# Optimization experiments

Hardware: AMD Instinct MI355X
Metric: run time of the kernel (lower is better)

The kernel has to match this reference:

```python
import jax, jax.numpy as jnp
import numpy as np

N_NODES = 50000
N_EDGES = 1600000
NEG_SLOPE = 0.2


def setup_inputs() -> dict:
    key = jax.random.key(0)
    ks = jax.random.split(key, 11)
    s = 0.1  # small init scale
    return {
        "x": jax.random.normal(ks[0], (N_NODES, 128), dtype=jnp.float32),
        "edge_index": jax.random.randint(ks[1], (2, N_EDGES), 0, N_NODES, dtype=jnp.int64),
        "W1": jax.random.normal(ks[2], (128, 128), dtype=jnp.float32) * s,
        "att_src1": jax.random.normal(ks[3], (2, 64), dtype=jnp.float32) * s,
        "att_dst1": jax.random.normal(ks[4], (2, 64), dtype=jnp.float32) * s,
        "b1": jax.random.normal(ks[5], (128,), dtype=jnp.float32) * s,
        "W2": jax.random.normal(ks[6], (128, 64), dtype=jnp.float32) * s,
        "att_src2": jax.random.normal(ks[7], (1, 64), dtype=jnp.float32) * s,
        "att_dst2": jax.random.normal(ks[8], (1, 64), dtype=jnp.float32) * s,
        "b2": jax.random.normal(ks[9], (64,), dtype=jnp.float32) * s,
    }


def gat_conv(x, W, a_src, a_dst, bias, src, dst, n_nodes):
    # x: [N, F_in]; W: [F_in, H*C]; a_src/a_dst: [H, C]; bias: [H*C]
    H, C = a_src.shape
    xl = (x @ W).reshape(n_nodes, H, C)                 # [N,H,C]
    alpha_s = jnp.einsum('nhc,hc->nh', xl, a_src)       # [N,H]
    alpha_d = jnp.einsum('nhc,hc->nh', xl, a_dst)       # [N,H]
    e = jax.nn.leaky_relu(alpha_s[src] + alpha_d[dst], NEG_SLOPE)  # [E,H]
    # segment softmax over edges sharing the same destination node
    m = jax.ops.segment_max(e, dst, num_segments=n_nodes)          # [N,H]
    m = jnp.where(jnp.isfinite(m), m, 0.0)
    e = jnp.exp(e - m[dst])
    denom = jax.ops.segment_sum(e, dst, num_segments=n_nodes)      # [N,H]
    alpha = e / denom[dst]                               # self-loops guarantee denom > 0
    msg = xl[src] * alpha[:, :, None]                    # [E,H,C]
    out = jax.ops.segment_sum(msg, dst, num_segments=n_nodes)      # [N,H,C]
    return out.reshape(n_nodes, H * C) + bias


def reference(x, edge_index, W1, att_src1, att_dst1, b1, W2, att_src2, att_dst2, b2):
    n = x.shape[0]
    # PyG GATConv default add_self_loops=True
    loops = jnp.arange(n, dtype=edge_index.dtype)
    src = jnp.concatenate([edge_index[0], loops])
    dst = jnp.concatenate([edge_index[1], loops])

    h = gat_conv(x, W1, att_src1, att_dst1, b1, src, dst, n)   # [N, 128]
    h = jax.nn.relu(h)                                          # dropout p=0 (eval)
    h = gat_conv(h, W2, att_src2, att_dst2, b2, src, dst, n)   # [N, 64]
    h = jax.nn.relu(h)
    return h
```

## Files before the change

kernel.cpp:

```cpp
#include <hip/hip_runtime.h>
#include <cstdint>
#include <cstddef>

#define NEG_SLOPE 0.2f

#define NB 512
#define LOG_NB 9
#define MAXK 512

__device__ inline unsigned short f2bf(float f) {
    unsigned int u = __float_as_uint(f);
    u += 0x7FFFu + ((u >> 16) & 1u);
    return (unsigned short)(u >> 16);
}
__device__ inline float bf_lo(unsigned int u) { return __uint_as_float(u << 16); }
__device__ inline float bf_hi(unsigned int u) { return __uint_as_float(u & 0xFFFF0000u); }
__device__ inline unsigned int pk2bf(float lo, float hi) {
    return (unsigned int)f2bf(lo) | ((unsigned int)f2bf(hi) << 16);
}

__global__ __launch_bounds__(256) void sort_count_kernel(const int* __restrict__ ei, int E,
                                                         int K, int CH, int* __restrict__ bcnt) {
    __shared__ int hist[MAXK];
    int tid = threadIdx.x;
    for (int i = tid; i < K; i += 256) hist[i] = 0;
    __syncthreads();
    int lo = blockIdx.x * CH;
    int hi = lo + CH; if (hi > E) hi = E;
    for (int e = lo + tid; e < hi; e += 256)
        atomicAdd(&hist[ei[(size_t)E + e] >> LOG_NB], 1);
    __syncthreads();
    for (int i = tid; i < K; i += 256)
        if (hist[i]) atomicAdd(&bcnt[i], hist[i]);
}

__global__ void sort_scan_kernel(const int* __restrict__ bcnt, int* __restrict__ boff,
                                 int* __restrict__ bcur, int K, int E) {
    __shared__ int buf[MAXK];
    int tid = threadIdx.x;
    int v = (tid < K) ? bcnt[tid] : 0;
    buf[tid] = v;
    __syncthreads();
    for (int o = 1; o < MAXK; o <<= 1) {
        int t = (tid >= o) ? buf[tid - o] : 0;
        __syncthreads();
        buf[tid] += t;
        __syncthreads();
    }
    if (tid < K) {
        int ex = buf[tid] - v;
        boff[tid] = ex;
        bcur[tid] = ex;
    }
    if (tid == K) boff[K] = E;
}

__global__ __launch_bounds__(256) void sort_scatter_kernel(const int* __restrict__ ei, int E,
                                                           int K, int CH, int* __restrict__ bcur,
                                                           unsigned int* __restrict__ bkt) {
    __shared__ int hist[MAXK];
    __shared__ int base[MAXK];
    int tid = threadIdx.x;
    for (int i = tid; i < K; i += 256) hist[i] = 0;
    __syncthreads();
    int lo = blockIdx.x * CH;
    int hi = lo + CH; if (hi > E) hi = E;
    for (int e = lo + tid; e < hi; e += 256)
        atomicAdd(&hist[ei[(size_t)E + e] >> LOG_NB], 1);
    __syncthreads();
    for (int i = tid; i < K; i += 256) {
        int c = hist[i];
        base[i] = c ? atomicAdd(&bcur[i], c) : 0;
    }
    __syncthreads();
    for (int i = tid; i < K; i += 256) hist[i] = 0;
    __syncthreads();
    for (int e = lo + tid; e < hi; e += 256) {
        int s = ei[e];
        int d = ei[(size_t)E + e];
        int k = d >> LOG_NB;
        int r = atomicAdd(&hist[k], 1);
        bkt[(size_t)base[k] + r] = (unsigned int)s | ((unsigned int)d << 16);
    }
}

__global__ __launch_bounds__(256) void sort_finalize_kernel(const unsigned int* __restrict__ bkt,
                                                            const int* __restrict__ boff,
                                                            int* __restrict__ off,
                                                            unsigned int* __restrict__ csrc, int N) {
    __shared__ int nhist[NB];
    __shared__ int part[256];
    __shared__ int loff[NB];
    int k = blockIdx.x;
    int tid = threadIdx.x;
    int node0 = k << LOG_NB;
    int nh = N - node0; if (nh > NB) nh = NB;
    int beg = boff[k], end = boff[k + 1];
    for (int i = tid; i < NB; i += 256) nhist[i] = 0;
    __syncthreads();
    for (int e = beg + tid; e < end; e += 256)
        atomicAdd(&nhist[(bkt[e] >> 16) - node0], 1);
    __syncthreads();
    int i0 = 2 * tid, i1 = 2 * tid + 1;
    int v0 = (i0 < nh) ? nhist[i0] + 1 : 0;
    int v1 = (i1 < nh) ? nhist[i1] + 1 : 0;
    part[tid] = v0 + v1;
    __syncthreads();
    for (int o = 1; o < 256; o <<= 1) {
        int t = (tid >= o) ? part[tid - o] : 0;
        __syncthreads();
        part[tid] += t;
        __syncthreads();
    }
    int gbase = beg + node0;
    int base = gbase + ((tid > 0) ? part[tid - 1] : 0);
    if (i0 < nh) loff[i0] = base;
    if (i1 < nh) loff[i1] = base + v0;
    __syncthreads();
    for (int i = tid; i < nh; i += 256) {
        int node = node0 + i;
        off[node] = loff[i];
        csrc[loff[i]] = (unsigned int)node | ((unsigned int)node << 16);
        nhist[i] = loff[i] + 1;
    }
    if (node0 + nh == N && tid == 0) off[N] = gbase + part[255];
    __syncthreads();
    for (int e = beg + tid; e < end; e += 256) {
        unsigned int p = bkt[e];
        int pos = atomicAdd(&nhist[(p >> 16) - node0], 1);
        csrc[pos] = p;
    }
}


template <int FOUT, int H, bool BF16IN>
__global__ __launch_bounds__(256) void gemm_att_kernel(const void* __restrict__ Xv,
                                                       const float* __restrict__ W,
                                                       const float* __restrict__ attS,
                                                       const float* __restrict__ attD,
                                                       unsigned short* __restrict__ Ybf,
                                                       float* __restrict__ as_,
                                                       float* __restrict__ ad_, int N) {
    constexpr int ROWS = 8192 / FOUT;
    constexpr int CG   = FOUT / 4;
    __shared__ float sX[ROWS][68];
    __shared__ float sW[64 * FOUT];
    int tid = threadIdx.x;
    int rowbase = blockIdx.x * ROWS;
    int cg = tid % CG;
    int rg = tid / CG;
    int r0 = rg * 8;

    float acc[8][4];
#pragma unroll
    for (int i = 0; i < 8; i++)
#pragma unroll
        for (int c = 0; c < 4; c++) acc[i][c] = 0.f;

    for (int k0 = 0; k0 < 128; k0 += 64) {
        __syncthreads();
        if (BF16IN) {
            const unsigned short* Xb = (const unsigned short*)Xv;
            for (int idx = tid; idx < ROWS * 8; idx += 256) {
                int r = idx >> 3, g = idx & 7;
                int row = rowbase + r;
                uint4 v = (row < N) ? *(const uint4*)&Xb[(size_t)row * 128 + k0 + g * 8]
                                    : make_uint4(0, 0, 0, 0);
                float* dst = &sX[r][g * 8];
                dst[0] = bf_lo(v.x); dst[1] = bf_hi(v.x);
                dst[2] = bf_lo(v.y); dst[3] = bf_hi(v.y);
                dst[4] = bf_lo(v.z); dst[5] = bf_hi(v.z);
                dst[6] = bf_lo(v.w); dst[7] = bf_hi(v.w);
            }
        } else {
            const float* X = (const float*)Xv;
            for (int idx = tid; idx < ROWS * 16; idx += 256) {
                int r = idx >> 4, q = idx & 15;
                int row = rowbase + r;
                float4 val = (row < N) ? *(const float4*)&X[(size_t)row * 128 + k0 + q * 4]
                                       : make_float4(0.f, 0.f, 0.f, 0.f);
                *(float4*)&sX[r][q * 4] = val;
            }
        }
        for (int idx = tid; idx < 16 * FOUT; idx += 256)
            *(float4*)&sW[idx * 4] = *(const float4*)&W[(size_t)k0 * FOUT + idx * 4];
        __syncthreads();
        for (int k = 0; k < 64; k += 4) {
            float4 xr[8];
#pragma unroll
            for (int i = 0; i < 8; i++)
                xr[i] = *(const float4*)&sX[r0 + i][k];
#pragma unroll
            for (int kk = 0; kk < 4; kk++) {
                float4 wv = ((const float4*)(sW + (size_t)(k + kk) * FOUT))[cg];
#pragma unroll
                for (int i = 0; i < 8; i++) {
                    float xv = (&xr[i].x)[kk];
                    acc[i][0] = fmaf(xv, wv.x, acc[i][0]);
                    acc[i][1] = fmaf(xv, wv.y, acc[i][1]);
                    acc[i][2] = fmaf(xv, wv.z, acc[i][2]);
                    acc[i][3] = fmaf(xv, wv.w, acc[i][3]);
                }
            }
        }
    }

#pragma unroll
    for (int i = 0; i < 8; i++) {
        int row = rowbase + r0 + i;
        if (row < N) {
            ushort4 v;
            v.x = f2bf(acc[i][0]); v.y = f2bf(acc[i][1]);
            v.z = f2bf(acc[i][2]); v.w = f2bf(acc[i][3]);
            *(ushort4*)(Ybf + (size_t)row * FOUT + cg * 4) = v;
        }
    }

    float4 asv = ((const float4*)attS)[cg];
    float4 adv = ((const float4*)attD)[cg];
    int head = (H == 2) ? (cg >> 4) : 0;
#pragma unroll
    for (int i = 0; i < 8; i++) {
        float ps = acc[i][0] * asv.x + acc[i][1] * asv.y + acc[i][2] * asv.z + acc[i][3] * asv.w;
        float pd = acc[i][0] * adv.x + acc[i][1] * adv.y + acc[i][2] * adv.z + acc[i][3] * adv.w;
#pragma unroll
        for (int o = 1; o <= 8; o <<= 1) { ps += __shfl_xor(ps, o); pd += __shfl_xor(pd, o); }
        int row = rowbase + r0 + i;
        if ((tid & 15) == 0 && row < N) {
            as_[(size_t)row * H + head] = ps;
            ad_[(size_t)row * H + head] = pd;
        }
    }
}


__global__ __launch_bounds__(256) void agg1_kernel(const unsigned short* __restrict__ xl,
                                                   const float* __restrict__ as_,
                                                   const float* __restrict__ ad_,
                                                   const float* __restrict__ bias,
                                                   const int* __restrict__ off,
                                                   const unsigned int* __restrict__ csrc,
                                                   unsigned short* __restrict__ out, int N) {
    __shared__ float4 sps[4][64];
    int wiw  = threadIdx.x >> 6;
    int lane = threadIdx.x & 63;
    int node = blockIdx.x * 4 + wiw;
    if (node >= N) return;
    int beg = off[node], end = off[node + 1];
    int deg = end - beg;
    float2 adn = ((const float2*)ad_)[node];

    int cl  = lane & 15;
    int sub = lane >> 4;
    int hd1 = (cl >> 3) & 1;
    float acc[8];
#pragma unroll
    for (int i = 0; i < 8; i++) acc[i] = 0.f;
    const char* xbase = (const char*)xl + cl * 16;

    if (deg <= 64) {
        int so = 0;
        float t0 = -1e30f, t1 = -1e30f;
        if (lane < deg) {
            int s = (int)(csrc[beg + lane] & 0xFFFFu);
            so = s << 8;
            float2 asv = ((const float2*)as_)[s];
            t0 = asv.x + adn.x; t0 = t0 > 0.f ? t0 : NEG_SLOPE * t0;
            t1 = asv.y + adn.y; t1 = t1 > 0.f ? t1 : NEG_SLOPE * t1;
        }
        float m0 = t0, m1 = t1;
#pragma unroll
        for (int o = 32; o; o >>= 1) {
            m0 = fmaxf(m0, __shfl_xor(m0, o));
            m1 = fmaxf(m1, __shfl_xor(m1, o));
        }
        float e0 = (lane < deg) ? __expf(t0 - m0) : 0.f;
        float e1 = (lane < deg) ? __expf(t1 - m1) : 0.f;
        float s0 = e0, s1 = e1;
#pragma unroll
        for (int o = 32; o; o >>= 1) { s0 += __shfl_xor(s0, o); s1 += __shfl_xor(s1, o); }
        sps[wiw][lane] = make_float4(e0 / s0, e1 / s1, __int_as_float(so), 0.f);
        int iters = (deg + 3) >> 2;
#pragma unroll 8
        for (int j = 0; j < iters; j++) {
            float4 q = sps[wiw][j * 4 + sub];
            float a  = hd1 ? q.y : q.x;
            uint4 v  = *(const uint4*)(xbase + __float_as_int(q.z));
            acc[0] = fmaf(a, bf_lo(v.x), acc[0]); acc[1] = fmaf(a, bf_hi(v.x), acc[1]);
            acc[2] = fmaf(a, bf_lo(v.y), acc[2]); acc[3] = fmaf(a, bf_hi(v.y), acc[3]);
            acc[4] = fmaf(a, bf_lo(v.z), acc[4]); acc[5] = fmaf(a, bf_hi(v.z), acc[5]);
            acc[6] = fmaf(a, bf_lo(v.w), acc[6]); acc[7] = fmaf(a, bf_hi(v.w), acc[7]);
        }
    } else {
        float m0 = -1e30f, m1 = -1e30f;
        for (int b = beg; b < end; b += 64) {
            int e = b + lane;
            if (e < end) {
                int s = (int)(csrc[e] & 0xFFFFu);
                float2 asv = ((const float2*)as_)[s];
                float t0 = asv.x + adn.x; t0 = t0 > 0.f ? t0 : NEG_SLOPE * t0;
                float t1 = asv.y + adn.y; t1 = t1 > 0.f ? t1 : NEG_SLOPE * t1;
                m0 = fmaxf(m0, t0); m1 = fmaxf(m1, t1);
            }
        }
#pragma unroll
        for (int o = 32; o; o >>= 1) {
            m0 = fmaxf(m0, __shfl_xor(m0, o));
            m1 = fmaxf(m1, __shfl_xor(m1, o));
        }
        float s0 = 0.f, s1 = 0.f;
        for (int b = beg; b < end; b += 64) {
            int e = b + lane;
            if (e < end) {
                int s = (int)(csrc[e] & 0xFFFFu);
                float2 asv = ((const float2*)as_)[s];
                float t0 = asv.x + adn.x; t0 = t0 > 0.f ? t0 : NEG_SLOPE * t0;
                float t1 = asv.y + adn.y; t1 = t1 > 0.f ? t1 : NEG_SLOPE * t1;
                s0 += __expf(t0 - m0); s1 += __expf(t1 - m1);
            }
        }
#pragma unroll
        for (int o = 32; o; o >>= 1) { s0 += __shfl_xor(s0, o); s1 += __shfl_xor(s1, o); }
        float i0 = 1.f / s0, i1 = 1.f / s1;
        for (int b = beg; b < end; b += 64) {
            int cnt = end - b; if (cnt > 64) cnt = 64;
            float p0 = 0.f, p1 = 0.f; int so = 0;
            if (lane < cnt) {
                int s = (int)(csrc[b + lane] & 0xFFFFu);
                so = s << 8;
                float2 asv = ((const float2*)as_)[s];
                float t0 = asv.x + adn.x; t0 = t0 > 0.f ? t0 : NEG_SLOPE * t0;
                float t1 = asv.y + adn.y; t1 = t1 > 0.f ? t1 : NEG_SLOPE * t1;
                p0 = __expf(t0 - m0) * i0; p1 = __expf(t1 - m1) * i1;
            }
            sps[wiw][lane] = make_float4(p0, p1, __int_as_float(so), 0.f);
            int iters = (cnt + 3) >> 2;
#pragma unroll 8
            for (int j = 0; j < iters; j++) {
                float4 q = sps[wiw][j * 4 + sub];
                float a  = hd1 ? q.y : q.x;
                uint4 v  = *(const uint4*)(xbase + __float_as_int(q.z));
                acc[0] = fmaf(a, bf_lo(v.x), acc[0]); acc[1] = fmaf(a, bf_hi(v.x), acc[1]);
                acc[2] = fmaf(a, bf_lo(v.y), acc[2]); acc[3] = fmaf(a, bf_hi(v.y), acc[3]);
                acc[4] = fmaf(a, bf_lo(v.z), acc[4]); acc[5] = fmaf(a, bf_hi(v.z), acc[5]);
                acc[6] = fmaf(a, bf_lo(v.w), acc[6]); acc[7] = fmaf(a, bf_hi(v.w), acc[7]);
            }
        }
    }
#pragma unroll
    for (int o = 16; o <= 32; o <<= 1)
#pragma unroll
        for (int i = 0; i < 8; i++) acc[i] += __shfl_xor(acc[i], o);
    if (sub == 0) {
        const float* bp = bias + cl * 8;
        uint4 pk;
        float v0, v1;
        v0 = fmaxf(acc[0] + bp[0], 0.f); v1 = fmaxf(acc[1] + bp[1], 0.f); pk.x = pk2bf(v0, v1);
        v0 = fmaxf(acc[2] + bp[2], 0.f); v1 = fmaxf(acc[3] + bp[3], 0.f); pk.y = pk2bf(v0, v1);
        v0 = fmaxf(acc[4] + bp[4], 0.f); v1 = fmaxf(acc[5] + bp[5], 0.f); pk.z = pk2bf(v0, v1);
        v0 = fmaxf(acc[6] + bp[6], 0.f); v1 = fmaxf(acc[7] + bp[7], 0.f); pk.w = pk2bf(v0, v1);
        *(uint4*)(out + (size_t)node * 128 + cl * 8) = pk;
    }
}


__global__ __launch_bounds__(256) void agg2_kernel(const unsigned short* __restrict__ xl,
                                                   const float* __restrict__ as_,
                                                   const float* __restrict__ ad_,
                                                   const float* __restrict__ bias,
                                                   const int* __restrict__ off,
                                                   const unsigned int* __restrict__ csrc,
                                                   float* __restrict__ out, int N) {
    __shared__ float2 sps[4][64];
    int wiw  = threadIdx.x >> 6;
    int lane = threadIdx.x & 63;
    int node = blockIdx.x * 4 + wiw;
    if (node >= N) return;
    int beg = off[node], end = off[node + 1];
    int deg = end - beg;
    float adn = ad_[node];

    int cl  = lane & 7;
    int sub = lane >> 3;
    float acc[8];
#pragma unroll
    for (int i = 0; i < 8; i++) acc[i] = 0.f;
    const char* xbase = (const char*)xl + cl * 16;

    if (deg <= 64) {
        int so = 0;
        float t = -1e30f;
        if (lane < deg) {
            int s = (int)(csrc[beg + lane] & 0xFFFFu);
            so = s << 7;
            t = as_[s] + adn;
            t = t > 0.f ? t : NEG_SLOPE * t;
        }
        float m = t;
#pragma unroll
        for (int o = 32; o; o >>= 1) m = fmaxf(m, __shfl_xor(m, o));
        float evv = (lane < deg) ? __expf(t - m) : 0.f;
        float sum = evv;
#pragma unroll
        for (int o = 32; o; o >>= 1) sum += __shfl_xor(sum, o);
        sps[wiw][lane] = make_float2(evv / sum, __int_as_float(so));
        int iters = (deg + 7) >> 3;
#pragma unroll 8
        for (int j = 0; j < iters; j++) {
            float2 q = sps[wiw][j * 8 + sub];
            float a  = q.x;
            uint4 v  = *(const uint4*)(xbase + __float_as_int(q.y));
            acc[0] = fmaf(a, bf_lo(v.x), acc[0]); acc[1] = fmaf(a, bf_hi(v.x), acc[1]);
            acc[2] = fmaf(a, bf_lo(v.y), acc[2]); acc[3] = fmaf(a, bf_hi(v.y), acc[3]);
            acc[4] = fmaf(a, bf_lo(v.z), acc[4]); acc[5] = fmaf(a, bf_hi(v.z), acc[5]);
            acc[6] = fmaf(a, bf_lo(v.w), acc[6]); acc[7] = fmaf(a, bf_hi(v.w), acc[7]);
        }
    } else {
        float m = -1e30f;
        for (int b = beg; b < end; b += 64) {
            int e = b + lane;
            if (e < end) {
                float t = as_[csrc[e] & 0xFFFFu] + adn;
                t = t > 0.f ? t : NEG_SLOPE * t;
                m = fmaxf(m, t);
            }
        }
#pragma unroll
        for (int o = 32; o; o >>= 1) m = fmaxf(m, __shfl_xor(m, o));
        float sum = 0.f;
        for (int b = beg; b < end; b += 64) {
            int e = b + lane;
            if (e < end) {
                float t = as_[csrc[e] & 0xFFFFu] + adn;
                t = t > 0.f ? t : NEG_SLOPE * t;
                sum += __expf(t - m);
            }
        }
#pragma unroll
        for (int o = 32; o; o >>= 1) sum += __shfl_xor(sum, o);
        float inv = 1.f / sum;
        for (int b = beg; b < end; b += 64) {
            int cnt = end - b; if (cnt > 64) cnt = 64;
            float p = 0.f; int so = 0;
            if (lane < cnt) {
                int s = (int)(csrc[b + lane] & 0xFFFFu);
                so = s << 7;
                float t = as_[s] + adn;
                t = t > 0.f ? t : NEG_SLOPE * t;
                p = __expf(t - m) * inv;
            }
            sps[wiw][lane] = make_float2(p, __int_as_float(so));
            int iters = (cnt + 7) >> 3;
#pragma unroll 8
            for (int j = 0; j < iters; j++) {
                float2 q = sps[wiw][j * 8 + sub];
                float a  = q.x;
                uint4 v  = *(const uint4*)(xbase + __float_as_int(q.y));
                acc[0] = fmaf(a, bf_lo(v.x), acc[0]); acc[1] = fmaf(a, bf_hi(v.x), acc[1]);
                acc[2] = fmaf(a, bf_lo(v.y), acc[2]); acc[3] = fmaf(a, bf_hi(v.y), acc[3]);
                acc[4] = fmaf(a, bf_lo(v.z), acc[4]); acc[5] = fmaf(a, bf_hi(v.z), acc[5]);
                acc[6] = fmaf(a, bf_lo(v.w), acc[6]); acc[7] = fmaf(a, bf_hi(v.w), acc[7]);
            }
        }
    }
#pragma unroll
    for (int o = 8; o <= 32; o <<= 1)
#pragma unroll
        for (int i = 0; i < 8; i++) acc[i] += __shfl_xor(acc[i], o);
    if (sub == 0) {
        float* op = out + (size_t)node * 64 + cl * 8;
        const float* bp = bias + cl * 8;
#pragma unroll
        for (int i = 0; i < 8; i++) op[i] = fmaxf(acc[i] + bp[i], 0.f);
    }
}


extern "C" void kernel_launch(void* const* d_in, const int* in_sizes, int n_in,
                              void* d_out, int out_size, void* d_ws, size_t ws_size,
                              hipStream_t stream) {
    const float* x        = (const float*)d_in[0];
    const int*   ei       = (const int*)d_in[1];
    const float* W1       = (const float*)d_in[2];
    const float* attS1    = (const float*)d_in[3];
    const float* attD1    = (const float*)d_in[4];
    const float* b1       = (const float*)d_in[5];
    const float* W2       = (const float*)d_in[6];
    const float* attS2    = (const float*)d_in[7];
    const float* attD2    = (const float*)d_in[8];
    const float* b2       = (const float*)d_in[9];
    float* out            = (float*)d_out;

    int N  = in_sizes[0] / 128;
    int E  = in_sizes[1] / 2;
    int EE = E + N;
    int K  = (N + NB - 1) >> LOG_NB;

    char* w = (char*)d_ws;
    auto alloc = [&](size_t bytes) -> void* {
        void* p = (void*)w;
        w += (bytes + 255) & ~(size_t)255;
        return p;
    };
    int*   bcnt = (int*)alloc((size_t)(K + 1) * 4);
    int*   boff = (int*)alloc((size_t)(K + 1) * 4);
    int*   bcur = (int*)alloc((size_t)(K + 1) * 4);
    int*   off  = (int*)alloc((size_t)(N + 1) * 4);
    unsigned int* csrc = (unsigned int*)alloc((size_t)EE * 4);
    unsigned short* xl1 = (unsigned short*)alloc((size_t)N * 128 * 2);
    float* sd1  = (float*)alloc((size_t)N * 2 * 4);
    float* dd1  = (float*)alloc((size_t)N * 2 * 4);
    unsigned short* h1 = (unsigned short*)alloc((size_t)N * 128 * 2);

    unsigned int* bkt = (unsigned int*)xl1;
    unsigned short* xl2 = xl1;
    float* sd2 = sd1;
    float* dd2 = dd1;

    hipMemsetAsync(bcnt, 0, (size_t)(K + 1) * 4, stream);

    int G  = 256;
    int CH = (E + G - 1) / G;
    sort_count_kernel<<<G, 256, 0, stream>>>(ei, E, K, CH, bcnt);
    sort_scan_kernel<<<1, MAXK, 0, stream>>>(bcnt, boff, bcur, K, E);
    sort_scatter_kernel<<<G, 256, 0, stream>>>(ei, E, K, CH, bcur, bkt);
    sort_finalize_kernel<<<K, 256, 0, stream>>>(bkt, boff, off, csrc, N);

    gemm_att_kernel<128, 2, false><<<(N + 63) / 64, 256, 0, stream>>>(x, W1, attS1, attD1, xl1, sd1, dd1, N);
    agg1_kernel<<<(N + 3) / 4, 256, 0, stream>>>(xl1, sd1, dd1, b1, off, csrc, h1, N);

    gemm_att_kernel<64, 1, true><<<(N + 127) / 128, 256, 0, stream>>>(h1, W2, attS2, attD2, xl2, sd2, dd2, N);
    agg2_kernel<<<(N + 3) / 4, 256, 0, stream>>>(xl2, sd2, dd2, b2, off, csrc, out, N);
}
```

Baseline: 341.3 us.

## Fuse edge scatter with layer-1 GEMM in one launch; store h1 as fp32

Merges the bucket-scatter sort pass and the first GEMM+attention projection into one kernel launch. Blocks below G do the scatter and the remaining blocks do the GEMM, so the two independent stages overlap on the GPU. This needs a separate bkt buffer, since it can no longer alias xl1. The layer-1 output h1 is now written as fp32 instead of bf16, removing the pack/unpack conversion but doubling h1 write and read traffic.

```diff
diff --git a/kernel.cpp b/kernel.cpp
--- a/kernel.cpp
+++ b/kernel.cpp
@@ -15,9 +15,6 @@
 }
 __device__ inline float bf_lo(unsigned int u) { return __uint_as_float(u << 16); }
 __device__ inline float bf_hi(unsigned int u) { return __uint_as_float(u & 0xFFFF0000u); }
-__device__ inline unsigned int pk2bf(float lo, float hi) {
-    return (unsigned int)f2bf(lo) | ((unsigned int)f2bf(hi) << 16);
-}
 
 __global__ __launch_bounds__(256) void sort_count_kernel(const int* __restrict__ ei, int E,
                                                          int K, int CH, int* __restrict__ bcnt) {
@@ -55,33 +52,145 @@
     if (tid == K) boff[K] = E;
 }
 
-__global__ __launch_bounds__(256) void sort_scatter_kernel(const int* __restrict__ ei, int E,
-                                                           int K, int CH, int* __restrict__ bcur,
-                                                           unsigned int* __restrict__ bkt) {
-    __shared__ int hist[MAXK];
-    __shared__ int base[MAXK];
+
+template <int FOUT, int H>
+__device__ __forceinline__ void gemm_att_body(const float* __restrict__ X,
+                                              const float* __restrict__ W,
+                                              const float* __restrict__ attS,
+                                              const float* __restrict__ attD,
+                                              unsigned short* __restrict__ Ybf,
+                                              float* __restrict__ as_,
+                                              float* __restrict__ ad_, int N, int bid,
+                                              float* sX, float* sW) {
+    constexpr int ROWS = 8192 / FOUT;
+    constexpr int CG   = FOUT / 4;
+    constexpr int LDX  = 68;
     int tid = threadIdx.x;
-    for (int i = tid; i < K; i += 256) hist[i] = 0;
-    __syncthreads();
-    int lo = blockIdx.x * CH;
-    int hi = lo + CH; if (hi > E) hi = E;
-    for (int e = lo + tid; e < hi; e += 256)
-        atomicAdd(&hist[ei[(size_t)E + e] >> LOG_NB], 1);
-    __syncthreads();
-    for (int i = tid; i < K; i += 256) {
-        int c = hist[i];
-        base[i] = c ? atomicAdd(&bcur[i], c) : 0;
-    }
-    __syncthreads();
-    for (int i = tid; i < K; i += 256) hist[i] = 0;
-    __syncthreads();
-    for (int e = lo + tid; e < hi; e += 256) {
-        int s = ei[e];
-        int d = ei[(size_t)E + e];
-        int k = d >> LOG_NB;
-        int r = atomicAdd(&hist[k], 1);
-        bkt[(size_t)base[k] + r] = (unsigned int)s | ((unsigned int)d << 16);
-    }
+    int rowbase = bid * ROWS;
+    int cg = tid % CG;
+    int rg = tid / CG;
+    int r0 = rg * 8;
+
+    float acc[8][4];
+#pragma unroll
+    for (int i = 0; i < 8; i++)
+#pragma unroll
+        for (int c = 0; c < 4; c++) acc[i][c] = 0.f;
+
+    for (int k0 = 0; k0 < 128; k0 += 64) {
+        __syncthreads();
+        for (int idx = tid; idx < ROWS * 16; idx += 256) {
+            int r = idx >> 4, q = idx & 15;
+            int row = rowbase + r;
+            float4 val = (row < N) ? *(const float4*)&X[(size_t)row * 128 + k0 + q * 4]
+                                   : make_float4(0.f, 0.f, 0.f, 0.f);
+            *(float4*)&sX[r * LDX + q * 4] = val;
+        }
+        for (int idx = tid; idx < 16 * FOUT; idx += 256)
+            *(float4*)&sW[idx * 4] = *(const float4*)&W[(size_t)k0 * FOUT + idx * 4];
+        __syncthreads();
+        for (int k = 0; k < 64; k += 4) {
+            float4 xr[8];
+#pragma unroll
+            for (int i = 0; i < 8; i++)
+                xr[i] = *(const float4*)&sX[(r0 + i) * LDX + k];
+#pragma unroll
+            for (int kk = 0; kk < 4; kk++) {
+                float4 wv = ((const float4*)(sW + (size_t)(k + kk) * FOUT))[cg];
+#pragma unroll
+                for (int i = 0; i < 8; i++) {
+                    float xv = (&xr[i].x)[kk];
+                    acc[i][0] = fmaf(xv, wv.x, acc[i][0]);
+                    acc[i][1] = fmaf(xv, wv.y, acc[i][1]);
+                    acc[i][2] = fmaf(xv, wv.z, acc[i][2]);
+                    acc[i][3] = fmaf(xv, wv.w, acc[i][3]);
+                }
+            }
+        }
+    }
+
+#pragma unroll
+    for (int i = 0; i < 8; i++) {
+        int row = rowbase + r0 + i;
+        if (row < N) {
+            ushort4 v;
+            v.x = f2bf(acc[i][0]); v.y = f2bf(acc[i][1]);
+            v.z = f2bf(acc[i][2]); v.w = f2bf(acc[i][3]);
+            *(ushort4*)(Ybf + (size_t)row * FOUT + cg * 4) = v;
+        }
+    }
+
+    float4 asv = ((const float4*)attS)[cg];
+    float4 adv = ((const float4*)attD)[cg];
+    int head = (H == 2) ? (cg >> 4) : 0;
+#pragma unroll
+    for (int i = 0; i < 8; i++) {
+        float ps = acc[i][0] * asv.x + acc[i][1] * asv.y + acc[i][2] * asv.z + acc[i][3] * asv.w;
+        float pd = acc[i][0] * adv.x + acc[i][1] * adv.y + acc[i][2] * adv.z + acc[i][3] * adv.w;
+#pragma unroll
+        for (int o = 1; o <= 8; o <<= 1) { ps += __shfl_xor(ps, o); pd += __shfl_xor(pd, o); }
+        int row = rowbase + r0 + i;
+        if ((tid & 15) == 0 && row < N) {
+            as_[(size_t)row * H + head] = ps;
+            ad_[(size_t)row * H + head] = pd;
+        }
+    }
+}
+
+__global__ __launch_bounds__(256) void scatter_gemm1_kernel(const int* __restrict__ ei, int E,
+                                                            int K, int CH, int* __restrict__ bcur,
+                                                            unsigned int* __restrict__ bkt,
+                                                            const float* __restrict__ X,
+                                                            const float* __restrict__ W1,
+                                                            const float* __restrict__ attS,
+                                                            const float* __restrict__ attD,
+                                                            unsigned short* __restrict__ Ybf,
+                                                            float* __restrict__ as_,
+                                                            float* __restrict__ ad_, int N, int G) {
+    __shared__ float sX[64 * 68];
+    __shared__ float sW[64 * 128];
+    if (blockIdx.x < G) {
+        int* hist = (int*)sW;
+        int* base = hist + MAXK;
+        int tid = threadIdx.x;
+        for (int i = tid; i < K; i += 256) hist[i] = 0;
+        __syncthreads();
+        int lo = blockIdx.x * CH;
+        int hi = lo + CH; if (hi > E) hi = E;
+        for (int e = lo + tid; e < hi; e += 256)
+            atomicAdd(&hist[ei[(size_t)E + e] >> LOG_NB], 1);
+        __syncthreads();
+        for (int i = tid; i < K; i += 256) {
+            int c = hist[i];
+            base[i] = c ? atomicAdd(&bcur[i], c) : 0;
+        }
+        __syncthreads();
+        for (int i = tid; i < K; i += 256) hist[i] = 0;
+        __syncthreads();
+        for (int e = lo + tid; e < hi; e += 256) {
+            int s = ei[e];
+            int d = ei[(size_t)E + e];
+            int k = d >> LOG_NB;
+            int r = atomicAdd(&hist[k], 1);
+            bkt[(size_t)base[k] + r] = (unsigned int)s | ((unsigned int)d << 16);
+        }
+    } else {
+        gemm_att_body<128, 2>(X, W1, attS, attD, Ybf, as_, ad_, N, blockIdx.x - G, sX, sW);
+    }
+}
+
+template <int FOUT, int H>
+__global__ __launch_bounds__(256) void gemm_att_kernel(const float* __restrict__ X,
+                                                       const float* __restrict__ W,
+                                                       const float* __restrict__ attS,
+                                                       const float* __restrict__ attD,
+                                                       unsigned short* __restrict__ Ybf,
+                                                       float* __restrict__ as_,
+                                                       float* __restrict__ ad_, int N) {
+    constexpr int ROWS = 8192 / FOUT;
+    __shared__ float sX[ROWS * 68];
+    __shared__ float sW[64 * FOUT];
+    gemm_att_body<FOUT, H>(X, W, attS, attD, Ybf, as_, ad_, N, blockIdx.x, sX, sW);
 }
 
 __global__ __launch_bounds__(256) void sort_finalize_kernel(const unsigned int* __restrict__ bkt,
@@ -133,114 +242,13 @@
 }
 
 
-template <int FOUT, int H, bool BF16IN>
-__global__ __launch_bounds__(256) void gemm_att_kernel(const void* __restrict__ Xv,
-                                                       const float* __restrict__ W,
-                                                       const float* __restrict__ attS,
-                                                       const float* __restrict__ attD,
-                                                       unsigned short* __restrict__ Ybf,
-                                                       float* __restrict__ as_,
-                                                       float* __restrict__ ad_, int N) {
-    constexpr int ROWS = 8192 / FOUT;
-    constexpr int CG   = FOUT / 4;
-    __shared__ float sX[ROWS][68];
-    __shared__ float sW[64 * FOUT];
-    int tid = threadIdx.x;
-    int rowbase = blockIdx.x * ROWS;
-    int cg = tid % CG;
-    int rg = tid / CG;
-    int r0 = rg * 8;
-
-    float acc[8][4];
-#pragma unroll
-    for (int i = 0; i < 8; i++)
-#pragma unroll
-        for (int c = 0; c < 4; c++) acc[i][c] = 0.f;
-
-    for (int k0 = 0; k0 < 128; k0 += 64) {
-        __syncthreads();
-        if (BF16IN) {
-            const unsigned short* Xb = (const unsigned short*)Xv;
-            for (int idx = tid; idx < ROWS * 8; idx += 256) {
-                int r = idx >> 3, g = idx & 7;
-                int row = rowbase + r;
-                uint4 v = (row < N) ? *(const uint4*)&Xb[(size_t)row * 128 + k0 + g * 8]
-                                    : make_uint4(0, 0, 0, 0);
-                float* dst = &sX[r][g * 8];
-                dst[0] = bf_lo(v.x); dst[1] = bf_hi(v.x);
-                dst[2] = bf_lo(v.y); dst[3] = bf_hi(v.y);
-                dst[4] = bf_lo(v.z); dst[5] = bf_hi(v.z);
-                dst[6] = bf_lo(v.w); dst[7] = bf_hi(v.w);
-            }
-        } else {
-            const float* X = (const float*)Xv;
-            for (int idx = tid; idx < ROWS * 16; idx += 256) {
-                int r = idx >> 4, q = idx & 15;
-                int row = rowbase + r;
-                float4 val = (row < N) ? *(const float4*)&X[(size_t)row * 128 + k0 + q * 4]
-                                       : make_float4(0.f, 0.f, 0.f, 0.f);
-                *(float4*)&sX[r][q * 4] = val;
-            }
-        }
-        for (int idx = tid; idx < 16 * FOUT; idx += 256)
-            *(float4*)&sW[idx * 4] = *(const float4*)&W[(size_t)k0 * FOUT + idx * 4];
-        __syncthreads();
-        for (int k = 0; k < 64; k += 4) {
-            float4 xr[8];
-#pragma unroll
-            for (int i = 0; i < 8; i++)
-                xr[i] = *(const float4*)&sX[r0 + i][k];
-#pragma unroll
-            for (int kk = 0; kk < 4; kk++) {
-                float4 wv = ((const float4*)(sW + (size_t)(k + kk) * FOUT))[cg];
-#pragma unroll
-                for (int i = 0; i < 8; i++) {
-                    float xv = (&xr[i].x)[kk];
-                    acc[i][0] = fmaf(xv, wv.x, acc[i][0]);
-                    acc[i][1] = fmaf(xv, wv.y, acc[i][1]);
-                    acc[i][2] = fmaf(xv, wv.z, acc[i][2]);
-                    acc[i][3] = fmaf(xv, wv.w, acc[i][3]);
-                }
-            }
-        }
-    }
-
-#pragma unroll
-    for (int i = 0; i < 8; i++) {
-        int row = rowbase + r0 + i;
-        if (row < N) {
-            ushort4 v;
-            v.x = f2bf(acc[i][0]); v.y = f2bf(acc[i][1]);
-            v.z = f2bf(acc[i][2]); v.w = f2bf(acc[i][3]);
-            *(ushort4*)(Ybf + (size_t)row * FOUT + cg * 4) = v;
-        }
-    }
-
-    float4 asv = ((const float4*)attS)[cg];
-    float4 adv = ((const float4*)attD)[cg];
-    int head = (H == 2) ? (cg >> 4) : 0;
-#pragma unroll
-    for (int i = 0; i < 8; i++) {
-        float ps = acc[i][0] * asv.x + acc[i][1] * asv.y + acc[i][2] * asv.z + acc[i][3] * asv.w;
-        float pd = acc[i][0] * adv.x + acc[i][1] * adv.y + acc[i][2] * adv.z + acc[i][3] * adv.w;
-#pragma unroll
-        for (int o = 1; o <= 8; o <<= 1) { ps += __shfl_xor(ps, o); pd += __shfl_xor(pd, o); }
-        int row = rowbase + r0 + i;
-        if ((tid & 15) == 0 && row < N) {
-            as_[(size_t)row * H + head] = ps;
-            ad_[(size_t)row * H + head] = pd;
-        }
-    }
-}
-
-
 __global__ __launch_bounds__(256) void agg1_kernel(const unsigned short* __restrict__ xl,
                                                    const float* __restrict__ as_,
                                                    const float* __restrict__ ad_,
                                                    const float* __restrict__ bias,
                                                    const int* __restrict__ off,
                                                    const unsigned int* __restrict__ csrc,
-                                                   unsigned short* __restrict__ out, int N) {
+                                                   float* __restrict__ out, int N) {
     __shared__ float4 sps[4][64];
     int wiw  = threadIdx.x >> 6;
     int lane = threadIdx.x & 63;
@@ -352,14 +360,10 @@
 #pragma unroll
         for (int i = 0; i < 8; i++) acc[i] += __shfl_xor(acc[i], o);
     if (sub == 0) {
+        float* op = out + (size_t)node * 128 + cl * 8;
         const float* bp = bias + cl * 8;
-        uint4 pk;
-        float v0, v1;
-        v0 = fmaxf(acc[0] + bp[0], 0.f); v1 = fmaxf(acc[1] + bp[1], 0.f); pk.x = pk2bf(v0, v1);
-        v0 = fmaxf(acc[2] + bp[2], 0.f); v1 = fmaxf(acc[3] + bp[3], 0.f); pk.y = pk2bf(v0, v1);
-        v0 = fmaxf(acc[4] + bp[4], 0.f); v1 = fmaxf(acc[5] + bp[5], 0.f); pk.z = pk2bf(v0, v1);
-        v0 = fmaxf(acc[6] + bp[6], 0.f); v1 = fmaxf(acc[7] + bp[7], 0.f); pk.w = pk2bf(v0, v1);
-        *(uint4*)(out + (size_t)node * 128 + cl * 8) = pk;
+#pragma unroll
+        for (int i = 0; i < 8; i++) op[i] = fmaxf(acc[i] + bp[i], 0.f);
     }
 }
 
@@ -507,28 +511,29 @@
     int*   bcur = (int*)alloc((size_t)(K + 1) * 4);
     int*   off  = (int*)alloc((size_t)(N + 1) * 4);
     unsigned int* csrc = (unsigned int*)alloc((size_t)EE * 4);
+    unsigned int* bkt  = (unsigned int*)alloc((size_t)E * 4);
     unsigned short* xl1 = (unsigned short*)alloc((size_t)N * 128 * 2);
     float* sd1  = (float*)alloc((size_t)N * 2 * 4);
     float* dd1  = (float*)alloc((size_t)N * 2 * 4);
-    unsigned short* h1 = (unsigned short*)alloc((size_t)N * 128 * 2);
-
-    unsigned int* bkt = (unsigned int*)xl1;
+    float* h1   = (float*)alloc((size_t)N * 128 * 4);
+
     unsigned short* xl2 = xl1;
     float* sd2 = sd1;
     float* dd2 = dd1;
 
     hipMemsetAsync(bcnt, 0, (size_t)(K + 1) * 4, stream);
 
-    int G  = 256;
-    int CH = (E + G - 1) / G;
+    int G   = 256;
+    int CH  = (E + G - 1) / G;
+    int GB1 = (N + 63) / 64;
     sort_count_kernel<<<G, 256, 0, stream>>>(ei, E, K, CH, bcnt);
     sort_scan_kernel<<<1, MAXK, 0, stream>>>(bcnt, boff, bcur, K, E);
-    sort_scatter_kernel<<<G, 256, 0, stream>>>(ei, E, K, CH, bcur, bkt);
+    scatter_gemm1_kernel<<<G + GB1, 256, 0, stream>>>(ei, E, K, CH, bcur, bkt,
+                                                      x, W1, attS1, attD1, xl1, sd1, dd1, N, G);
     sort_finalize_kernel<<<K, 256, 0, stream>>>(bkt, boff, off, csrc, N);
 
-    gemm_att_kernel<128, 2, false><<<(N + 63) / 64, 256, 0, stream>>>(x, W1, attS1, attD1, xl1, sd1, dd1, N);
     agg1_kernel<<<(N + 3) / 4, 256, 0, stream>>>(xl1, sd1, dd1, b1, off, csrc, h1, N);
 
-    gemm_att_kernel<64, 1, true><<<(N + 127) / 128, 256, 0, stream>>>(h1, W2, attS2, attD2, xl2, sd2, dd2, N);
+    gemm_att_kernel<64, 1><<<(N + 127) / 128, 256, 0, stream>>>(h1, W2, attS2, attD2, xl2, sd2, dd2, N);
     agg2_kernel<<<(N + 3) / 4, 256, 0, stream>>>(xl2, sd2, dd2, b2, off, csrc, out, N);
 }
```

Result: faster. 326.9 us (-4.2%).
